# Kernel optimization log

Hardware: AMD Instinct MI355X
Metric: run time of the kernel (lower is better)

## Reference

```python
import jax, jax.numpy as jnp
import numpy as np

N_STATE = 1280
N_HEAD = 20
HEAD_DIM = 64  # hardcoded in the original module
B = 1          # batch hardcoded to 1 by reshape in qkv_attention
N_CTX = 32
CACHE = 16384


def setup_inputs() -> dict:
    key = jax.random.key(0)
    ks = jax.random.split(key, 11)
    s = 0.02  # param init scale
    return {
        "x": jax.random.normal(ks[0], (B, N_CTX, N_STATE), jnp.float32),
        "self_k_cache": jax.random.normal(ks[1], (B, CACHE, N_STATE), jnp.float32),
        "self_v_cache": jax.random.normal(ks[2], (B, CACHE, N_STATE), jnp.float32),
        "positions": jnp.arange(N_CTX, dtype=jnp.int64) if jax.config.jax_enable_x64 else jnp.arange(N_CTX, dtype=jnp.int32),
        "mask": jnp.zeros((N_CTX, CACHE), jnp.float32),
        # learned parameters (Linear stores weight as [out, in]; y = x @ W.T + b)
        "Wq": jax.random.normal(ks[3], (N_STATE, N_STATE), jnp.float32) * s,
        "bq": jax.random.normal(ks[4], (N_STATE,), jnp.float32) * s,
        "Wk": jax.random.normal(ks[5], (N_STATE, N_STATE), jnp.float32) * s,  # key has no bias
        "Wv": jax.random.normal(ks[6], (N_STATE, N_STATE), jnp.float32) * s,
        "bv": jax.random.normal(ks[7], (N_STATE,), jnp.float32) * s,
        "Wout": jax.random.normal(ks[8], (N_STATE, N_STATE), jnp.float32) * s,
        "bout": jax.random.normal(ks[9], (N_STATE,), jnp.float32) * s,
    }


def reference(x, self_k_cache, self_v_cache, positions, mask,
              Wq, bq, Wk, Wv, bv, Wout, bout):
    scale2 = HEAD_DIM ** -0.5
    # projections
    q = x @ Wq.T + bq          # [B, n_ctx, n_state]
    k = x @ Wk.T               # [B, n_ctx, n_state] (no bias)
    v = x @ Wv.T + bv
    # scatter KV-cache update: self_k_cache[:, positions, :] = k
    kc = self_k_cache.at[:, positions, :].set(k)   # [B, CACHE, n_state]
    vc = self_v_cache.at[:, positions, :].set(v)
    # split heads
    qh = q.reshape(B, N_CTX, N_HEAD, HEAD_DIM).transpose(0, 2, 1, 3)  # [B,H,q,d]
    kh = kc.reshape(B, CACHE, N_HEAD, HEAD_DIM)                        # [B,k,H,d]
    vh = vc.reshape(B, CACHE, N_HEAD, HEAD_DIM)
    # attention: softmax(q k^T * scale2 + mask) v
    qk = jnp.einsum('bhqd,bkhd->bhqk', qh, kh) * scale2 + mask         # [B,H,q,k]
    w = jax.nn.softmax(qk, axis=-1)
    o = jnp.einsum('bhqk,bkhd->bqhd', w, vh).reshape(1, N_CTX, N_HEAD * HEAD_DIM)
    out = o @ Wout.T + bout
    return out, kc, vc
```

## Files before the change

kernel.cpp:

```cpp
#include <hip/hip_runtime.h>
#include <hip/hip_bf16.h>

#define H 20
#define Q 32
#define D 64
#define NSTATE 1280
#define CACHE_N 16384
#define NSPLIT 32
#define KCHUNK (CACHE_N / NSPLIT)
#define TK 64

__device__ __forceinline__ void gemm_body(const float* __restrict__ x,
                                          const float* __restrict__ W,
                                          const float* __restrict__ bias,
                                          float* __restrict__ out,
                                          int c0, int ksplit) {
    __shared__ float xs[64][36];
    __shared__ float ws[64][66];
    const int t = threadIdx.x;
    const int rt = t >> 5;
    const int ct = t & 31;
    float acc[4][2] = {};

    const int kbeg = ksplit * 320;
#pragma unroll 1
    for (int k0 = kbeg; k0 < kbeg + 320; k0 += 64) {
        __syncthreads();
#pragma unroll
        for (int p = 0; p < 2; ++p) {
            int idx = t + p * 256;
            int row = idx >> 4, c4 = idx & 15;
            float4 v4 = *(const float4*)(x + row * NSTATE + k0 + c4 * 4);
            xs[c4 * 4 + 0][row] = v4.x; xs[c4 * 4 + 1][row] = v4.y;
            xs[c4 * 4 + 2][row] = v4.z; xs[c4 * 4 + 3][row] = v4.w;
        }
#pragma unroll
        for (int p = 0; p < 4; ++p) {
            int idx = t + p * 256;
            int c = idx >> 4, c4 = idx & 15;
            float4 v4 = *(const float4*)(W + (long long)(c0 + c) * NSTATE + k0 + c4 * 4);
            ws[c4 * 4 + 0][c] = v4.x; ws[c4 * 4 + 1][c] = v4.y;
            ws[c4 * 4 + 2][c] = v4.z; ws[c4 * 4 + 3][c] = v4.w;
        }
        __syncthreads();
#pragma unroll 8
        for (int kk = 0; kk < 64; ++kk) {
            float4 xv = *(const float4*)&xs[kk][rt * 4];
            float2 wv = *(const float2*)&ws[kk][ct * 2];
            acc[0][0] += xv.x * wv.x; acc[0][1] += xv.x * wv.y;
            acc[1][0] += xv.y * wv.x; acc[1][1] += xv.y * wv.y;
            acc[2][0] += xv.z * wv.x; acc[2][1] += xv.z * wv.y;
            acc[3][0] += xv.w * wv.x; acc[3][1] += xv.w * wv.y;
        }
    }
#pragma unroll
    for (int r = 0; r < 4; ++r) {
        int i = rt * 4 + r;
#pragma unroll
        for (int cc = 0; cc < 2; ++cc) {
            int c = c0 + ct * 2 + cc;
            float val = acc[r][cc];
            if (ksplit == 0 && bias) val += bias[c];
            atomicAdd(&out[i * NSTATE + c], val);
        }
    }
}

__global__ __launch_bounds__(256, 2)
void gemm_qkv(const float* __restrict__ x,
              const float* __restrict__ Wq, const float* __restrict__ bq,
              const float* __restrict__ Wk,
              const float* __restrict__ Wv, const float* __restrict__ bv,
              float* __restrict__ q, float* __restrict__ k, float* __restrict__ v) {
    const int mat = blockIdx.z;
    const float* W; const float* bias; float* out;
    if (mat == 0)      { W = Wq; bias = bq;      out = q; }
    else if (mat == 1) { W = Wk; bias = nullptr; out = k; }
    else               { W = Wv; bias = bv;      out = v; }
    gemm_body(x, W, bias, out, blockIdx.x * 64, blockIdx.y);
}

__global__ __launch_bounds__(256, 2)
void gemm_one(const float* __restrict__ x, const float* __restrict__ W,
              const float* __restrict__ bias, float* __restrict__ out) {
    gemm_body(x, W, bias, out, blockIdx.x * 64, blockIdx.y);
}

__global__ void build_rowmap(const int* __restrict__ pos, int* __restrict__ rowmap) {
    int i = threadIdx.x;
    if (i < Q) rowmap[pos[i]] = i;
}

__global__ __launch_bounds__(256, 2)
void attn_fused(const float* __restrict__ qw,
                const float* __restrict__ kci, const float* __restrict__ vci,
                const float* __restrict__ knew, const float* __restrict__ vnew,
                const int* __restrict__ rowmap, const float* __restrict__ mask,
                float* __restrict__ kc, float* __restrict__ vc,
                float* __restrict__ mpart, float* __restrict__ lpart,
                __hip_bfloat16* __restrict__ opart) {
    const int h  = blockIdx.y;
    const int sp = blockIdx.x;
    const int j_base = sp * KCHUNK;

    __shared__ float qs[D][36];
    __shared__ float ks_[D][66];
    __shared__ float vs[TK][68];
    __shared__ float ps[TK][36];
    __shared__ float m_s[Q], l_s[Q], alpha_s[Q], tmax[Q], tsum[Q];

    const int t = threadIdx.x;
    const int qt = t >> 5;
    const int kt = t & 31;
    const int dt = t & 31;

#pragma unroll
    for (int p = 0; p < 2; ++p) {
        int idx = t + p * 256;
        int i = idx >> 4, c4 = idx & 15;
        float4 v4 = *(const float4*)(qw + i * NSTATE + h * D + c4 * 4);
        const float sc = 0.125f;
        qs[c4 * 4 + 0][i] = v4.x * sc; qs[c4 * 4 + 1][i] = v4.y * sc;
        qs[c4 * 4 + 2][i] = v4.z * sc; qs[c4 * 4 + 3][i] = v4.w * sc;
    }
    if (t < Q) { m_s[t] = -1e30f; l_s[t] = 0.f; }
    float oacc[4][2] = {};
    __syncthreads();

#pragma unroll 1
    for (int tile = 0; tile < KCHUNK / TK; ++tile) {
        const int j0 = j_base + tile * TK;
        __syncthreads();
#pragma unroll
        for (int p = 0; p < 4; ++p) {
            int idx = t + p * 256;
            int row = idx >> 4, c4 = idx & 15;
            long long j = j0 + row;
            int src = rowmap[j];
            const float* kb; const float* vb;
            if (src >= 0) { kb = knew + (long long)src * NSTATE; vb = vnew + (long long)src * NSTATE; }
            else          { kb = kci + j * NSTATE;               vb = vci + j * NSTATE; }
            float4 k4 = *(const float4*)(kb + h * D + c4 * 4);
            float4 v4 = *(const float4*)(vb + h * D + c4 * 4);
            *(float4*)(kc + j * NSTATE + h * D + c4 * 4) = k4;
            *(float4*)(vc + j * NSTATE + h * D + c4 * 4) = v4;
            ks_[c4 * 4 + 0][row] = k4.x; ks_[c4 * 4 + 1][row] = k4.y;
            ks_[c4 * 4 + 2][row] = k4.z; ks_[c4 * 4 + 3][row] = k4.w;
            *(float4*)&vs[row][c4 * 4] = v4;
        }
        __syncthreads();

        float s[4][2] = {};
#pragma unroll 8
        for (int d = 0; d < D; ++d) {
            float4 qv = *(const float4*)&qs[d][qt * 4];
            float2 kv = *(const float2*)&ks_[d][kt * 2];
            s[0][0] += qv.x * kv.x; s[0][1] += qv.x * kv.y;
            s[1][0] += qv.y * kv.x; s[1][1] += qv.y * kv.y;
            s[2][0] += qv.z * kv.x; s[2][1] += qv.z * kv.y;
            s[3][0] += qv.w * kv.x; s[3][1] += qv.w * kv.y;
        }
#pragma unroll
        for (int r = 0; r < 4; ++r) {
            int i = qt * 4 + r;
            float2 mv = *(const float2*)(mask + (long long)i * CACHE_N + j0 + kt * 2);
            s[r][0] += mv.x; s[r][1] += mv.y;
        }
        float rmax[4];
#pragma unroll
        for (int r = 0; r < 4; ++r) rmax[r] = fmaxf(s[r][0], s[r][1]);
#pragma unroll
        for (int off = 16; off >= 1; off >>= 1)
#pragma unroll
            for (int r = 0; r < 4; ++r)
                rmax[r] = fmaxf(rmax[r], __shfl_xor(rmax[r], off, 64));
        if (kt == 0)
#pragma unroll
            for (int r = 0; r < 4; ++r) tmax[qt * 4 + r] = rmax[r];
        __syncthreads();
        if (t < Q) {
            float mo = m_s[t], mn = fmaxf(mo, tmax[t]);
            float a = __expf(mo - mn);
            m_s[t] = mn; alpha_s[t] = a; l_s[t] *= a;
        }
        __syncthreads();
        float pr[4][2], rsum[4];
#pragma unroll
        for (int r = 0; r < 4; ++r) {
            float mn = m_s[qt * 4 + r];
            pr[r][0] = __expf(s[r][0] - mn);
            pr[r][1] = __expf(s[r][1] - mn);
            rsum[r] = pr[r][0] + pr[r][1];
        }
#pragma unroll
        for (int c = 0; c < 2; ++c)
            *(float4*)&ps[kt * 2 + c][qt * 4] =
                make_float4(pr[0][c], pr[1][c], pr[2][c], pr[3][c]);
#pragma unroll
        for (int off = 16; off >= 1; off >>= 1)
#pragma unroll
            for (int r = 0; r < 4; ++r)
                rsum[r] += __shfl_xor(rsum[r], off, 64);
        if (kt == 0)
#pragma unroll
            for (int r = 0; r < 4; ++r) tsum[qt * 4 + r] = rsum[r];
        {
            float a0 = alpha_s[qt * 4 + 0], a1 = alpha_s[qt * 4 + 1];
            float a2 = alpha_s[qt * 4 + 2], a3 = alpha_s[qt * 4 + 3];
            oacc[0][0] *= a0; oacc[0][1] *= a0;
            oacc[1][0] *= a1; oacc[1][1] *= a1;
            oacc[2][0] *= a2; oacc[2][1] *= a2;
            oacc[3][0] *= a3; oacc[3][1] *= a3;
        }
        __syncthreads();
        if (t < Q) l_s[t] += tsum[t];
#pragma unroll 8
        for (int j = 0; j < TK; ++j) {
            float4 pv = *(const float4*)&ps[j][qt * 4];
            float2 vv = *(const float2*)&vs[j][dt * 2];
            oacc[0][0] += pv.x * vv.x; oacc[0][1] += pv.x * vv.y;
            oacc[1][0] += pv.y * vv.x; oacc[1][1] += pv.y * vv.y;
            oacc[2][0] += pv.z * vv.x; oacc[2][1] += pv.z * vv.y;
            oacc[3][0] += pv.w * vv.x; oacc[3][1] += pv.w * vv.y;
        }
    }
    __syncthreads();
    const int pb = (h * NSPLIT + sp) * Q;
    if (t < Q) { mpart[pb + t] = m_s[t]; lpart[pb + t] = l_s[t]; }
#pragma unroll
    for (int r = 0; r < 4; ++r) {
        int i = qt * 4 + r;
        __hip_bfloat16 hx = __float2bfloat16(oacc[r][0]);
        __hip_bfloat16 hy = __float2bfloat16(oacc[r][1]);
        ushort2 u = make_ushort2(*(unsigned short*)&hx, *(unsigned short*)&hy);
        *(ushort2*)((unsigned short*)opart + (size_t)(pb + i) * D + dt * 2) = u;
    }
}

__global__ __launch_bounds__(64)
void attn_combine(const float* __restrict__ mpart, const float* __restrict__ lpart,
                  const __hip_bfloat16* __restrict__ opart, float* __restrict__ oattn) {
    const int i = blockIdx.x;
    const int h = blockIdx.y;
    const int d = threadIdx.x;
    float m[NSPLIT];
    float gm = -1e30f;
#pragma unroll
    for (int s = 0; s < NSPLIT; ++s) {
        m[s] = mpart[(h * NSPLIT + s) * Q + i];
        gm = fmaxf(gm, m[s]);
    }
    float l = 0.f, o = 0.f;
#pragma unroll
    for (int s = 0; s < NSPLIT; ++s) {
        float w = __expf(m[s] - gm);
        l += lpart[(h * NSPLIT + s) * Q + i] * w;
        o += __bfloat162float(opart[(size_t)((h * NSPLIT + s) * Q + i) * D + d]) * w;
    }
    oattn[i * NSTATE + h * D + d] = o / l;
}

extern "C" void kernel_launch(void* const* d_in, const int* in_sizes, int n_in,
                              void* d_out, int out_size, void* d_ws, size_t ws_size,
                              hipStream_t stream) {
    const float* x    = (const float*)d_in[0];
    const float* kci  = (const float*)d_in[1];
    const float* vci  = (const float*)d_in[2];
    const int*   pos  = (const int*)d_in[3];
    const float* mask = (const float*)d_in[4];
    const float* Wq   = (const float*)d_in[5];
    const float* bq   = (const float*)d_in[6];
    const float* Wk   = (const float*)d_in[7];
    const float* Wv   = (const float*)d_in[8];
    const float* bv   = (const float*)d_in[9];
    const float* Wout = (const float*)d_in[10];
    const float* bout = (const float*)d_in[11];

    float* out  = (float*)d_out;
    float* kc   = out + 40960;
    float* vc   = kc + CACHE_N * NSTATE;

    float* ws      = (float*)d_ws;
    float* kws     = ws;
    float* vws     = ws + 40960;
    float* qws     = ws + 81920;
    float* mpart   = ws + 122880;
    float* lpart   = ws + 143360;
    int*   rowmap  = (int*)(ws + 163840);
    __hip_bfloat16* opart = (__hip_bfloat16*)(ws + 180224);
    float* oattn   = qws;

    hipMemsetAsync(ws, 0, 3 * 40960 * sizeof(float), stream);
    hipMemsetAsync(out, 0, 40960 * sizeof(float), stream);
    hipMemsetAsync(rowmap, 0xFF, CACHE_N * sizeof(int), stream);

    build_rowmap<<<1, 64, 0, stream>>>(pos, rowmap);

    gemm_qkv<<<dim3(NSTATE / 64, 4, 3), 256, 0, stream>>>(x, Wq, bq, Wk, Wv, bv, qws, kws, vws);

    attn_fused<<<dim3(NSPLIT, H), 256, 0, stream>>>(qws, kci, vci, kws, vws, rowmap, mask,
                                                    kc, vc, mpart, lpart, opart);

    attn_combine<<<dim3(Q, H), 64, 0, stream>>>(mpart, lpart, opart, oattn);

    gemm_one<<<dim3(NSTATE / 64, 4), 256, 0, stream>>>(oattn, Wout, bout, out);
}
```

Measured before the change: 406.0 us.

## Prefetch next tiles into registers and keep softmax stats per-thread in attention

Both the projection GEMM and the fused attention kernel now load the next K/V (or x/W) tile into registers while computing on the current shared-memory tile. The attention kernel also keeps the online-softmax max and sum per row in registers, computed with wavefront shuffles, which removes two block barriers and the shared stat arrays per tile. It writes the cache copy with nontemporal stores and raises the occupancy hint to three blocks per SM. The change adds register pressure and always loads the old cache row even when a new row replaces it.

```diff
diff --git a/kernel.cpp b/kernel.cpp
--- a/kernel.cpp
+++ b/kernel.cpp
@@ -9,6 +9,9 @@
 #define NSPLIT 32
 #define KCHUNK (CACHE_N / NSPLIT)
 #define TK 64
+#define NTILE (KCHUNK / TK)
+
+typedef float f32x4 __attribute__((ext_vector_type(4)));
 
 __device__ __forceinline__ void gemm_body(const float* __restrict__ x,
                                           const float* __restrict__ W,
@@ -23,6 +26,21 @@
     float acc[4][2] = {};
 
     const int kbeg = ksplit * 320;
+
+    float4 xv[2], wv[4];
+#pragma unroll
+    for (int p = 0; p < 2; ++p) {
+        int idx = t + p * 256;
+        int row = idx >> 4, c4 = idx & 15;
+        xv[p] = *(const float4*)(x + row * NSTATE + kbeg + c4 * 4);
+    }
+#pragma unroll
+    for (int p = 0; p < 4; ++p) {
+        int idx = t + p * 256;
+        int c = idx >> 4, c4 = idx & 15;
+        wv[p] = *(const float4*)(W + (long long)(c0 + c) * NSTATE + kbeg + c4 * 4);
+    }
+
 #pragma unroll 1
     for (int k0 = kbeg; k0 < kbeg + 320; k0 += 64) {
         __syncthreads();
@@ -30,27 +48,40 @@
         for (int p = 0; p < 2; ++p) {
             int idx = t + p * 256;
             int row = idx >> 4, c4 = idx & 15;
-            float4 v4 = *(const float4*)(x + row * NSTATE + k0 + c4 * 4);
-            xs[c4 * 4 + 0][row] = v4.x; xs[c4 * 4 + 1][row] = v4.y;
-            xs[c4 * 4 + 2][row] = v4.z; xs[c4 * 4 + 3][row] = v4.w;
+            xs[c4 * 4 + 0][row] = xv[p].x; xs[c4 * 4 + 1][row] = xv[p].y;
+            xs[c4 * 4 + 2][row] = xv[p].z; xs[c4 * 4 + 3][row] = xv[p].w;
         }
 #pragma unroll
         for (int p = 0; p < 4; ++p) {
             int idx = t + p * 256;
             int c = idx >> 4, c4 = idx & 15;
-            float4 v4 = *(const float4*)(W + (long long)(c0 + c) * NSTATE + k0 + c4 * 4);
-            ws[c4 * 4 + 0][c] = v4.x; ws[c4 * 4 + 1][c] = v4.y;
-            ws[c4 * 4 + 2][c] = v4.z; ws[c4 * 4 + 3][c] = v4.w;
+            ws[c4 * 4 + 0][c] = wv[p].x; ws[c4 * 4 + 1][c] = wv[p].y;
+            ws[c4 * 4 + 2][c] = wv[p].z; ws[c4 * 4 + 3][c] = wv[p].w;
         }
         __syncthreads();
+        if (k0 + 64 < kbeg + 320) {
+            const int kn = k0 + 64;
+#pragma unroll
+            for (int p = 0; p < 2; ++p) {
+                int idx = t + p * 256;
+                int row = idx >> 4, c4 = idx & 15;
+                xv[p] = *(const float4*)(x + row * NSTATE + kn + c4 * 4);
+            }
+#pragma unroll
+            for (int p = 0; p < 4; ++p) {
+                int idx = t + p * 256;
+                int c = idx >> 4, c4 = idx & 15;
+                wv[p] = *(const float4*)(W + (long long)(c0 + c) * NSTATE + kn + c4 * 4);
+            }
+        }
 #pragma unroll 8
         for (int kk = 0; kk < 64; ++kk) {
-            float4 xv = *(const float4*)&xs[kk][rt * 4];
-            float2 wv = *(const float2*)&ws[kk][ct * 2];
-            acc[0][0] += xv.x * wv.x; acc[0][1] += xv.x * wv.y;
-            acc[1][0] += xv.y * wv.x; acc[1][1] += xv.y * wv.y;
-            acc[2][0] += xv.z * wv.x; acc[2][1] += xv.z * wv.y;
-            acc[3][0] += xv.w * wv.x; acc[3][1] += xv.w * wv.y;
+            float4 xq = *(const float4*)&xs[kk][rt * 4];
+            float2 wq = *(const float2*)&ws[kk][ct * 2];
+            acc[0][0] += xq.x * wq.x; acc[0][1] += xq.x * wq.y;
+            acc[1][0] += xq.y * wq.x; acc[1][1] += xq.y * wq.y;
+            acc[2][0] += xq.z * wq.x; acc[2][1] += xq.z * wq.y;
+            acc[3][0] += xq.w * wq.x; acc[3][1] += xq.w * wq.y;
         }
     }
 #pragma unroll
@@ -91,7 +122,7 @@
     if (i < Q) rowmap[pos[i]] = i;
 }
 
-__global__ __launch_bounds__(256, 2)
+__global__ __launch_bounds__(256, 3)
 void attn_fused(const float* __restrict__ qw,
                 const float* __restrict__ kci, const float* __restrict__ vci,
                 const float* __restrict__ knew, const float* __restrict__ vnew,
@@ -106,51 +137,90 @@
     __shared__ float qs[D][36];
     __shared__ float ks_[D][66];
     __shared__ float vs[TK][68];
-    __shared__ float ps[TK][36];
-    __shared__ float m_s[Q], l_s[Q], alpha_s[Q], tmax[Q], tsum[Q];
-
-    const int t = threadIdx.x;
+    __shared__ float ps2[Q][TK];
+
+    const int t  = threadIdx.x;
     const int qt = t >> 5;
     const int kt = t & 31;
-    const int dt = t & 31;
+    const int srow = t >> 4;
+    const int c4   = t & 15;
 
 #pragma unroll
     for (int p = 0; p < 2; ++p) {
         int idx = t + p * 256;
-        int i = idx >> 4, c4 = idx & 15;
-        float4 v4 = *(const float4*)(qw + i * NSTATE + h * D + c4 * 4);
+        int i = idx >> 4, cc = idx & 15;
+        float4 v4 = *(const float4*)(qw + i * NSTATE + h * D + cc * 4);
         const float sc = 0.125f;
-        qs[c4 * 4 + 0][i] = v4.x * sc; qs[c4 * 4 + 1][i] = v4.y * sc;
-        qs[c4 * 4 + 2][i] = v4.z * sc; qs[c4 * 4 + 3][i] = v4.w * sc;
-    }
-    if (t < Q) { m_s[t] = -1e30f; l_s[t] = 0.f; }
+        qs[cc * 4 + 0][i] = v4.x * sc; qs[cc * 4 + 1][i] = v4.y * sc;
+        qs[cc * 4 + 2][i] = v4.z * sc; qs[cc * 4 + 3][i] = v4.w * sc;
+    }
+
+    float m_r[4], l_r[4];
+#pragma unroll
+    for (int r = 0; r < 4; ++r) { m_r[r] = -1e30f; l_r[r] = 0.f; }
     float oacc[4][2] = {};
-    __syncthreads();
+
+    float4 ka[4], va[4];
+    float2 mk[4];
+    int    sr[4];
+    {
+        const int j0 = j_base;
+#pragma unroll
+        for (int p = 0; p < 4; ++p) {
+            int row = srow + 16 * p;
+            long long j = j0 + row;
+            sr[p] = rowmap[j];
+            ka[p] = *(const float4*)(kci + j * NSTATE + h * D + c4 * 4);
+            va[p] = *(const float4*)(vci + j * NSTATE + h * D + c4 * 4);
+        }
+#pragma unroll
+        for (int r = 0; r < 4; ++r)
+            mk[r] = *(const float2*)(mask + (long long)(qt * 4 + r) * CACHE_N + j0 + kt * 2);
+    }
 
 #pragma unroll 1
-    for (int tile = 0; tile < KCHUNK / TK; ++tile) {
+    for (int tile = 0; tile < NTILE; ++tile) {
         const int j0 = j_base + tile * TK;
         __syncthreads();
+
 #pragma unroll
         for (int p = 0; p < 4; ++p) {
-            int idx = t + p * 256;
-            int row = idx >> 4, c4 = idx & 15;
+            if (sr[p] >= 0) {
+                ka[p] = *(const float4*)(knew + (long long)sr[p] * NSTATE + h * D + c4 * 4);
+                va[p] = *(const float4*)(vnew + (long long)sr[p] * NSTATE + h * D + c4 * 4);
+            }
+        }
+#pragma unroll
+        for (int p = 0; p < 4; ++p) {
+            int row = srow + 16 * p;
             long long j = j0 + row;
-            int src = rowmap[j];
-            const float* kb; const float* vb;
-            if (src >= 0) { kb = knew + (long long)src * NSTATE; vb = vnew + (long long)src * NSTATE; }
-            else          { kb = kci + j * NSTATE;               vb = vci + j * NSTATE; }
-            float4 k4 = *(const float4*)(kb + h * D + c4 * 4);
-            float4 v4 = *(const float4*)(vb + h * D + c4 * 4);
-            *(float4*)(kc + j * NSTATE + h * D + c4 * 4) = k4;
-            *(float4*)(vc + j * NSTATE + h * D + c4 * 4) = v4;
-            ks_[c4 * 4 + 0][row] = k4.x; ks_[c4 * 4 + 1][row] = k4.y;
-            ks_[c4 * 4 + 2][row] = k4.z; ks_[c4 * 4 + 3][row] = k4.w;
-            *(float4*)&vs[row][c4 * 4] = v4;
+            __builtin_nontemporal_store(*(const f32x4*)&ka[p], (f32x4*)(kc + j * NSTATE + h * D + c4 * 4));
+            __builtin_nontemporal_store(*(const f32x4*)&va[p], (f32x4*)(vc + j * NSTATE + h * D + c4 * 4));
+            ks_[c4 * 4 + 0][row] = ka[p].x; ks_[c4 * 4 + 1][row] = ka[p].y;
+            ks_[c4 * 4 + 2][row] = ka[p].z; ks_[c4 * 4 + 3][row] = ka[p].w;
+            *(float4*)&vs[row][c4 * 4] = va[p];
         }
         __syncthreads();
 
-        float s[4][2] = {};
+        float s[4][2];
+#pragma unroll
+        for (int r = 0; r < 4; ++r) { s[r][0] = mk[r].x; s[r][1] = mk[r].y; }
+
+        if (tile + 1 < NTILE) {
+            const int jn = j0 + TK;
+#pragma unroll
+            for (int p = 0; p < 4; ++p) {
+                int row = srow + 16 * p;
+                long long j = jn + row;
+                sr[p] = rowmap[j];
+                ka[p] = *(const float4*)(kci + j * NSTATE + h * D + c4 * 4);
+                va[p] = *(const float4*)(vci + j * NSTATE + h * D + c4 * 4);
+            }
+#pragma unroll
+            for (int r = 0; r < 4; ++r)
+                mk[r] = *(const float2*)(mask + (long long)(qt * 4 + r) * CACHE_N + jn + kt * 2);
+        }
+
 #pragma unroll 8
         for (int d = 0; d < D; ++d) {
             float4 qv = *(const float4*)&qs[d][qt * 4];
@@ -160,12 +230,7 @@
             s[2][0] += qv.z * kv.x; s[2][1] += qv.z * kv.y;
             s[3][0] += qv.w * kv.x; s[3][1] += qv.w * kv.y;
         }
-#pragma unroll
-        for (int r = 0; r < 4; ++r) {
-            int i = qt * 4 + r;
-            float2 mv = *(const float2*)(mask + (long long)i * CACHE_N + j0 + kt * 2);
-            s[r][0] += mv.x; s[r][1] += mv.y;
-        }
+
         float rmax[4];
 #pragma unroll
         for (int r = 0; r < 4; ++r) rmax[r] = fmaxf(s[r][0], s[r][1]);
@@ -174,66 +239,67 @@
 #pragma unroll
             for (int r = 0; r < 4; ++r)
                 rmax[r] = fmaxf(rmax[r], __shfl_xor(rmax[r], off, 64));
-        if (kt == 0)
-#pragma unroll
-            for (int r = 0; r < 4; ++r) tmax[qt * 4 + r] = rmax[r];
-        __syncthreads();
-        if (t < Q) {
-            float mo = m_s[t], mn = fmaxf(mo, tmax[t]);
-            float a = __expf(mo - mn);
-            m_s[t] = mn; alpha_s[t] = a; l_s[t] *= a;
-        }
-        __syncthreads();
+
         float pr[4][2], rsum[4];
 #pragma unroll
         for (int r = 0; r < 4; ++r) {
-            float mn = m_s[qt * 4 + r];
+            float mn = fmaxf(m_r[r], rmax[r]);
+            float a  = __expf(m_r[r] - mn);
+            m_r[r]   = mn;
             pr[r][0] = __expf(s[r][0] - mn);
             pr[r][1] = __expf(s[r][1] - mn);
-            rsum[r] = pr[r][0] + pr[r][1];
-        }
-#pragma unroll
-        for (int c = 0; c < 2; ++c)
-            *(float4*)&ps[kt * 2 + c][qt * 4] =
-                make_float4(pr[0][c], pr[1][c], pr[2][c], pr[3][c]);
+            rsum[r]  = pr[r][0] + pr[r][1];
+            l_r[r]  *= a;
+            oacc[r][0] *= a; oacc[r][1] *= a;
+        }
 #pragma unroll
         for (int off = 16; off >= 1; off >>= 1)
 #pragma unroll
             for (int r = 0; r < 4; ++r)
                 rsum[r] += __shfl_xor(rsum[r], off, 64);
-        if (kt == 0)
-#pragma unroll
-            for (int r = 0; r < 4; ++r) tsum[qt * 4 + r] = rsum[r];
-        {
-            float a0 = alpha_s[qt * 4 + 0], a1 = alpha_s[qt * 4 + 1];
-            float a2 = alpha_s[qt * 4 + 2], a3 = alpha_s[qt * 4 + 3];
-            oacc[0][0] *= a0; oacc[0][1] *= a0;
-            oacc[1][0] *= a1; oacc[1][1] *= a1;
-            oacc[2][0] *= a2; oacc[2][1] *= a2;
-            oacc[3][0] *= a3; oacc[3][1] *= a3;
-        }
-        __syncthreads();
-        if (t < Q) l_s[t] += tsum[t];
-#pragma unroll 8
-        for (int j = 0; j < TK; ++j) {
-            float4 pv = *(const float4*)&ps[j][qt * 4];
-            float2 vv = *(const float2*)&vs[j][dt * 2];
-            oacc[0][0] += pv.x * vv.x; oacc[0][1] += pv.x * vv.y;
-            oacc[1][0] += pv.y * vv.x; oacc[1][1] += pv.y * vv.y;
-            oacc[2][0] += pv.z * vv.x; oacc[2][1] += pv.z * vv.y;
-            oacc[3][0] += pv.w * vv.x; oacc[3][1] += pv.w * vv.y;
-        }
-    }
-    __syncthreads();
+#pragma unroll
+        for (int r = 0; r < 4; ++r) l_r[r] += rsum[r];
+
+#pragma unroll
+        for (int r = 0; r < 4; ++r)
+            *(float2*)&ps2[qt * 4 + r][kt * 2] = make_float2(pr[r][0], pr[r][1]);
+
+#pragma unroll 4
+        for (int jb = 0; jb < TK; jb += 4) {
+            float4 pA = *(const float4*)&ps2[qt * 4 + 0][jb];
+            float4 pB = *(const float4*)&ps2[qt * 4 + 1][jb];
+            float4 pC = *(const float4*)&ps2[qt * 4 + 2][jb];
+            float4 pD = *(const float4*)&ps2[qt * 4 + 3][jb];
+            float pa0[4] = {pA.x, pA.y, pA.z, pA.w};
+            float pa1[4] = {pB.x, pB.y, pB.z, pB.w};
+            float pa2[4] = {pC.x, pC.y, pC.z, pC.w};
+            float pa3[4] = {pD.x, pD.y, pD.z, pD.w};
+#pragma unroll
+            for (int jj = 0; jj < 4; ++jj) {
+                float2 vv = *(const float2*)&vs[jb + jj][kt * 2];
+                oacc[0][0] += pa0[jj] * vv.x; oacc[0][1] += pa0[jj] * vv.y;
+                oacc[1][0] += pa1[jj] * vv.x; oacc[1][1] += pa1[jj] * vv.y;
+                oacc[2][0] += pa2[jj] * vv.x; oacc[2][1] += pa2[jj] * vv.y;
+                oacc[3][0] += pa3[jj] * vv.x; oacc[3][1] += pa3[jj] * vv.y;
+            }
+        }
+    }
+
     const int pb = (h * NSPLIT + sp) * Q;
-    if (t < Q) { mpart[pb + t] = m_s[t]; lpart[pb + t] = l_s[t]; }
+    if (kt == 0) {
+#pragma unroll
+        for (int r = 0; r < 4; ++r) {
+            mpart[pb + qt * 4 + r] = m_r[r];
+            lpart[pb + qt * 4 + r] = l_r[r];
+        }
+    }
 #pragma unroll
     for (int r = 0; r < 4; ++r) {
         int i = qt * 4 + r;
         __hip_bfloat16 hx = __float2bfloat16(oacc[r][0]);
         __hip_bfloat16 hy = __float2bfloat16(oacc[r][1]);
         ushort2 u = make_ushort2(*(unsigned short*)&hx, *(unsigned short*)&hy);
-        *(ushort2*)((unsigned short*)opart + (size_t)(pb + i) * D + dt * 2) = u;
+        *(ushort2*)((unsigned short*)opart + (size_t)(pb + i) * D + kt * 2) = u;
     }
 }
 
@@ -290,9 +356,9 @@
     __hip_bfloat16* opart = (__hip_bfloat16*)(ws + 180224);
     float* oattn   = qws;
 
-    hipMemsetAsync(ws, 0, 3 * 40960 * sizeof(float), stream);
-    hipMemsetAsync(out, 0, 40960 * sizeof(float), stream);
-    hipMemsetAsync(rowmap, 0xFF, CACHE_N * sizeof(int), stream);
+    (void)hipMemsetAsync(ws, 0, 3 * 40960 * sizeof(float), stream);
+    (void)hipMemsetAsync(out, 0, 40960 * sizeof(float), stream);
+    (void)hipMemsetAsync(rowmap, 0xFF, CACHE_N * sizeof(int), stream);
 
     build_rowmap<<<1, 64, 0, stream>>>(pos, rowmap);
 
```

New measurement: 396.6 us. 2.3% less time.
